# Kernel optimization log

Hardware: AMD Instinct MI355X
Metric: run time of the kernel (lower is better)

The kernel has to match this reference:

```python
import jax, jax.numpy as jnp
import numpy as np

# Kornia's fixed 5x5 pyramid (binomial) kernel used by build_pyramid/pyrdown
_PYR_K = np.array([[1, 4, 6, 4, 1],
                   [4, 16, 24, 16, 4],
                   [6, 24, 36, 24, 6],
                   [4, 16, 24, 16, 4],
                   [1, 4, 6, 4, 1]], dtype=np.float32) / 256.0


def _pyrdown(x):
    """kornia pyrdown: 5x5 binomial blur (reflect pad) + bilinear resize to (H//2, W//2)."""
    B, C, H, W = x.shape
    xp = jnp.pad(x, ((0, 0), (0, 0), (2, 2), (2, 2)), mode='reflect')
    k = jnp.broadcast_to(jnp.asarray(_PYR_K, x.dtype), (C, 1, 5, 5))  # depthwise
    y = jax.lax.conv_general_dilated(
        xp, k, window_strides=(1, 1), padding='VALID',
        feature_group_count=C, dimension_numbers=('NCHW', 'OIHW', 'NCHW'))
    # torch F.interpolate bilinear align_corners=False == jax resize bilinear, antialias off
    return jax.image.resize(y, (B, C, H // 2, W // 2), method='bilinear', antialias=False)


def _norm_pc(x):
    """Per-channel min-max normalization to [0,1] over spatial dims."""
    mx = jnp.max(x, axis=(2, 3), keepdims=True)
    mn = jnp.min(x, axis=(2, 3), keepdims=True)
    return (x - mn) / (mx - mn)


def _avg_local_max(x):
    """Mean of 16x16 tile maxima; torch loop range(0, H-16, 16) skips the last tile
    row/col, and with zero tiles the torch code yields nan_to_num(0/0) == 0."""
    B, C, H, W = x.shape
    s = 16
    ny = len(range(0, H - s, s))
    nx = len(range(0, W - s, s))
    if ny == 0 or nx == 0:
        return jnp.zeros((B, C, 1, 1), x.dtype)
    t = x[:, :, :ny * s, :nx * s].reshape(B, C, ny, s, nx, s)
    lmax = jnp.max(t, axis=(3, 5))           # [B,C,ny,nx]
    return jnp.mean(lmax, axis=(2, 3)).reshape(B, C, 1, 1)


def _sm_normalization(x):
    d = _norm_pc(x)
    lm = _avg_local_max(d)
    return d * (1.0 - lm) ** 2


def setup_inputs() -> dict:
    key = jax.random.key(0)
    x = jax.random.normal(key, (8, 3, 512, 512), dtype=jnp.float32)
    return {"x": x}


def reference(x):
    B, C, H, W = x.shape
    inp = _norm_pc(x)
    max_level = int(H).bit_length() - 1   # 9 for H=512
    u = max_level - 1

    # Gaussian pyramid of length max_level: [inp, pyrdown(inp), ...]
    pyr = [inp]
    for _ in range(max_level - 1):
        pyr.append(_pyrdown(pyr[-1]))

    acc = None
    for i in range(u - 1):
        h, w = pyr[i + 1].shape[2], pyr[i + 1].shape[3]
        up = jnp.repeat(jnp.repeat(pyr[i + 2], 2, axis=2), 2, axis=3)[:, :, :h, :w]
        d = jnp.abs(pyr[i + 1] - up)
        nd = jax.image.resize(_sm_normalization(d), (B, C, H, W),
                              method='bilinear', antialias=False)
        acc = nd if acc is None else acc + nd

    return jnp.mean(acc, axis=1)  # [B,H,W]
```

## Files before the change

kernel.cpp:

```cpp
#include <hip/hip_runtime.h>
#include <math.h>

#define NPLANES 24
#define FINF 3.402823466e38f

__host__ __device__ __forceinline__ int d_off(int li) {
    return 2097152 - (2097152 >> (2 * li));
}

__device__ __forceinline__ int refl(int v, int S) {
    if (v < 0) v = -v;
    if (v >= S) v = 2 * S - 2 - v;
    return v;
}

__device__ __forceinline__ float wmin64(float v) {
#pragma unroll
    for (int o = 32; o > 0; o >>= 1) v = fminf(v, __shfl_down(v, o, 64));
    return v;
}
__device__ __forceinline__ float wmax64(float v) {
#pragma unroll
    for (int o = 32; o > 0; o >>= 1) v = fmaxf(v, __shfl_down(v, o, 64));
    return v;
}
__device__ __forceinline__ float wsum64(float v) {
#pragma unroll
    for (int o = 32; o > 0; o >>= 1) v += __shfl_down(v, o, 64);
    return v;
}
__device__ __forceinline__ float bmin1024(float v, float* cross, int tid) {
    v = wmin64(v);
    if ((tid & 63) == 0) cross[tid >> 6] = v;
    __syncthreads();
    if (tid < 16) {
        float t = cross[tid];
#pragma unroll
        for (int o = 8; o > 0; o >>= 1) t = fminf(t, __shfl_down(t, o, 16));
        if (tid == 0) cross[0] = t;
    }
    __syncthreads();
    float r = cross[0];
    __syncthreads();
    return r;
}
__device__ __forceinline__ float bmax1024(float v, float* cross, int tid) {
    v = wmax64(v);
    if ((tid & 63) == 0) cross[tid >> 6] = v;
    __syncthreads();
    if (tid < 16) {
        float t = cross[tid];
#pragma unroll
        for (int o = 8; o > 0; o >>= 1) t = fmaxf(t, __shfl_down(t, o, 16));
        if (tid == 0) cross[0] = t;
    }
    __syncthreads();
    float r = cross[0];
    __syncthreads();
    return r;
}
__device__ __forceinline__ float bsum1024(float v, float* cross, int tid) {
    v = wsum64(v);
    if ((tid & 63) == 0) cross[tid >> 6] = v;
    __syncthreads();
    if (tid < 16) {
        float t = cross[tid];
#pragma unroll
        for (int o = 8; o > 0; o >>= 1) t += __shfl_down(t, o, 16);
        if (tid == 0) cross[0] = t;
    }
    __syncthreads();
    float r = cross[0];
    __syncthreads();
    return r;
}

__device__ __forceinline__ float stencil6(const float* s, int S, int i, int j) {
    const float w[6] = {1.f, 5.f, 10.f, 10.f, 5.f, 1.f};
    int rx[6];
#pragma unroll
    for (int b = 0; b < 6; ++b) rx[b] = refl(2 * j - 2 + b, S);
    float acc = 0.f;
#pragma unroll
    for (int a = 0; a < 6; ++a) {
        int ry = refl(2 * i - 2 + a, S);
        const float* rp = s + ry * S;
        float r = 0.f;
#pragma unroll
        for (int b = 0; b < 6; ++b) r += w[b] * rp[rx[b]];
        acc += w[a] * r;
    }
    return acc * (1.f / 1024.f);
}

template <int IS, bool HAS_D, int LI>
__global__ __launch_bounds__(256) void pyrdown_tiled(const float* __restrict__ in,
                                                     float* __restrict__ out,
                                                     float* __restrict__ dout,
                                                     float* __restrict__ tileMin,
                                                     float* __restrict__ tileMax) {
    constexpr int SO = IS / 2;
    constexpr int TO = 32;
    constexpr int TI = 2 * TO + 4;
    constexpr int TPA = SO / TO;
    __shared__ float sIn[TI * TI];
    __shared__ float sH[TI * TO];
    __shared__ float sOut[TO * TO];
    __shared__ float sD[HAS_D ? 64 * 65 : 1];
    __shared__ float rmn[HAS_D ? 256 : 1], rmx[HAS_D ? 256 : 1];

    const int tid = threadIdx.x;
    const int p = blockIdx.x / (TPA * TPA);
    const int t = blockIdx.x % (TPA * TPA);
    const int ty = t / TPA, tx = t % TPA;
    const int oy = ty * TO, ox = tx * TO;
    const int iy = 2 * oy - 2, ix = 2 * ox - 2;
    const float* ip = in + (size_t)p * IS * IS;

    for (int k = tid; k < TI * TI; k += 256) {
        int r = k / TI, c = k - r * TI;
        sIn[k] = ip[refl(iy + r, IS) * IS + refl(ix + c, IS)];
    }
    __syncthreads();

    for (int k = tid; k < TI * TO; k += 256) {
        int r = k / TO, j = k - r * TO;
        const float* rp = sIn + r * TI + 2 * j;
        sH[k] = rp[0] + 5.f * rp[1] + 10.f * rp[2] + 10.f * rp[3] + 5.f * rp[4] + rp[5];
    }
    __syncthreads();

    float* op = out + (size_t)p * SO * SO;
    for (int k = tid; k < TO * TO; k += 256) {
        int i = k / TO, j = k - i * TO;
        const float* cp = sH + (2 * i) * TO + j;
        float v = (cp[0] + 5.f * cp[TO] + 10.f * cp[2 * TO] + 10.f * cp[3 * TO] +
                   5.f * cp[4 * TO] + cp[5 * TO]) * (1.f / 1024.f);
        sOut[k] = v;
        op[(size_t)(oy + i) * SO + ox + j] = v;
    }

    if (HAS_D) {
        __syncthreads();
        float* dp = dout + (size_t)p * IS * IS;
        for (int k = tid; k < 4096; k += 256) {
            int yy = k >> 6, xx = k & 63;
            float dv = fabsf(sIn[(yy + 2) * TI + xx + 2] - sOut[(yy >> 1) * TO + (xx >> 1)]);
            sD[yy * 65 + xx] = dv;
            dp[(size_t)(2 * oy + yy) * IS + 2 * ox + xx] = dv;
        }
        __syncthreads();
        int s = tid >> 4, r = tid & 15;
        int tr = s >> 2, tc = s & 3;
        const float* rowp = sD + (tr * 16 + r) * 65 + tc * 16;
        float mn = FINF, mx = -FINF;
#pragma unroll
        for (int c = 0; c < 16; ++c) {
            float v = rowp[c];
            mn = fminf(mn, v); mx = fmaxf(mx, v);
        }
        rmn[tid] = mn; rmx[tid] = mx;
        __syncthreads();
        for (int st = 8; st > 0; st >>= 1) {
            if (r < st) {
                rmn[tid] = fminf(rmn[tid], rmn[tid + st]);
                rmx[tid] = fmaxf(rmx[tid], rmx[tid + st]);
            }
            __syncthreads();
        }
        if (r == 0) {
            constexpr int TA = IS / 16;
            constexpr int baseLi = (LI == 0) ? 0 : 6144;
            int gidx = baseLi + p * TA * TA + (ty * 4 + tr) * TA + (tx * 4 + tc);
            tileMin[gidx] = rmn[tid];
            tileMax[gidx] = rmx[tid];
        }
    }
}

__global__ __launch_bounds__(1024) void fused_small_kernel(const float* __restrict__ pyr3,
                                                           float* __restrict__ dBase,
                                                           const float* __restrict__ tileMin,
                                                           const float* __restrict__ tileMax,
                                                           float* __restrict__ A,
                                                           float* __restrict__ B) {
    __shared__ float sp3[4096], sd2[4096];
    __shared__ float sp4[1024], sd3[1024];
    __shared__ float sp5[256], sd4[256];
    __shared__ float sp6[64], sd5[64];
    __shared__ float sp7[16], sd6[16];
    __shared__ float cross[16];
    __shared__ float strip[256];
    __shared__ float tmaxLds[16];
    const int tid = threadIdx.x;
    const int p = blockIdx.x;

    ((float4*)sp3)[tid] = ((const float4*)(pyr3 + (size_t)p * 4096))[tid];
    __syncthreads();

    {
        float* d2g = dBase + d_off(2) + (size_t)p * 4096;
        int i = tid >> 5, j = tid & 31;
        float v = stencil6(sp3, 64, i, j);
        sp4[tid] = v;
#pragma unroll
        for (int di = 0; di < 2; ++di)
#pragma unroll
            for (int dj = 0; dj < 2; ++dj) {
                int y = 2 * i + di, x = 2 * j + dj;
                float dv = fabsf(sp3[y * 64 + x] - v);
                sd2[y * 64 + x] = dv;
                d2g[y * 64 + x] = dv;
            }
    }
    __syncthreads();
    if (tid < 256) {
        int i = tid >> 4, j = tid & 15;
        float v = stencil6(sp4, 32, i, j);
        sp5[tid] = v;
        float* d3g = dBase + d_off(3) + (size_t)p * 1024;
#pragma unroll
        for (int di = 0; di < 2; ++di)
#pragma unroll
            for (int dj = 0; dj < 2; ++dj) {
                int y = 2 * i + di, x = 2 * j + dj;
                float dv = fabsf(sp4[y * 32 + x] - v);
                sd3[y * 32 + x] = dv;
                d3g[y * 32 + x] = dv;
            }
    }
    __syncthreads();
    if (tid < 64) {
        int i = tid >> 3, j = tid & 7;
        float v = stencil6(sp5, 16, i, j);
        sp6[tid] = v;
        float* d4g = dBase + d_off(4) + (size_t)p * 256;
#pragma unroll
        for (int di = 0; di < 2; ++di)
#pragma unroll
            for (int dj = 0; dj < 2; ++dj) {
                int y = 2 * i + di, x = 2 * j + dj;
                float dv = fabsf(sp5[y * 16 + x] - v);
                sd4[y * 16 + x] = dv;
                d4g[y * 16 + x] = dv;
            }
    }
    __syncthreads();
    if (tid < 16) {
        int i = tid >> 2, j = tid & 3;
        float v = stencil6(sp6, 8, i, j);
        sp7[tid] = v;
        float* d5g = dBase + d_off(5) + (size_t)p * 64;
#pragma unroll
        for (int di = 0; di < 2; ++di)
#pragma unroll
            for (int dj = 0; dj < 2; ++dj) {
                int y = 2 * i + di, x = 2 * j + dj;
                float dv = fabsf(sp6[y * 8 + x] - v);
                sd5[y * 8 + x] = dv;
                d5g[y * 8 + x] = dv;
            }
    }
    __syncthreads();
    if (tid < 4) {
        int i = tid >> 1, j = tid & 1;
        float v = stencil6(sp7, 4, i, j);
        float* d6g = dBase + d_off(6) + (size_t)p * 16;
#pragma unroll
        for (int di = 0; di < 2; ++di)
#pragma unroll
            for (int dj = 0; dj < 2; ++dj) {
                int y = 2 * i + di, x = 2 * j + dj;
                float dv = fabsf(sp7[y * 4 + x] - v);
                sd6[y * 4 + x] = dv;
                d6g[y * 4 + x] = dv;
            }
    }
    __syncthreads();

    {
        float4 q = ((const float4*)sd2)[tid];
        float mn = fminf(fminf(q.x, q.y), fminf(q.z, q.w));
        float mx = fmaxf(fmaxf(q.x, q.y), fmaxf(q.z, q.w));
        mn = bmin1024(mn, cross, tid);
        mx = bmax1024(mx, cross, tid);
        if (tid < 256) {
            int t = tid >> 4, r = tid & 15;
            int ty = t >> 2, tx = t & 3;
            const float* rowp = sd2 + (ty * 16 + r) * 64 + tx * 16;
            float sm = -FINF;
#pragma unroll
            for (int c = 0; c < 16; ++c) sm = fmaxf(sm, rowp[c]);
            strip[tid] = sm;
        }
        __syncthreads();
        if (tid < 16) {
            float tm = -FINF;
            for (int r = 0; r < 16; ++r) tm = fmaxf(tm, strip[tid * 16 + r]);
            tmaxLds[tid] = tm;
        }
        __syncthreads();
        if (tid == 0) {
            float s = 0.f;
            for (int ty = 0; ty < 3; ++ty)
                for (int tx = 0; tx < 3; ++tx) s += tmaxLds[ty * 4 + tx];
            float inv = 1.f / (mx - mn);
            float lm = (s * (1.f / 9.f) - mn) * inv;
            float g = (1.f - lm) * (1.f - lm);
            A[2 * NPLANES + p] = g * inv;
            B[2 * NPLANES + p] = -mn * g * inv;
        }
        __syncthreads();
    }
    {
        float v = sd3[tid];
        float mn = bmin1024(v, cross, tid);
        float mx = bmax1024(v, cross, tid);
        float e = (tid < 256) ? sd3[(tid >> 4) * 32 + (tid & 15)] : -FINF;
        float tm = bmax1024(e, cross, tid);
        if (tid == 0) {
            float inv = 1.f / (mx - mn);
            float lm = (tm - mn) * inv;
            float g = (1.f - lm) * (1.f - lm);
            A[3 * NPLANES + p] = g * inv;
            B[3 * NPLANES + p] = -mn * g * inv;
        }
    }
    {
        float v = (tid < 256) ? sd4[tid] : FINF;
        float mn = bmin1024(v, cross, tid);
        v = (tid < 256) ? sd4[tid] : -FINF;
        float mx = bmax1024(v, cross, tid);
        if (tid == 0) {
            float inv = 1.f / (mx - mn);
            A[4 * NPLANES + p] = inv; B[4 * NPLANES + p] = -mn * inv;
        }
    }
    {
        float v = (tid < 64) ? sd5[tid] : FINF;
        float mn = bmin1024(v, cross, tid);
        v = (tid < 64) ? sd5[tid] : -FINF;
        float mx = bmax1024(v, cross, tid);
        if (tid == 0) {
            float inv = 1.f / (mx - mn);
            A[5 * NPLANES + p] = inv; B[5 * NPLANES + p] = -mn * inv;
        }
    }
    {
        float v = (tid < 16) ? sd6[tid] : FINF;
        float mn = bmin1024(v, cross, tid);
        v = (tid < 16) ? sd6[tid] : -FINF;
        float mx = bmax1024(v, cross, tid);
        if (tid == 0) {
            float inv = 1.f / (mx - mn);
            A[6 * NPLANES + p] = inv; B[6 * NPLANES + p] = -mn * inv;
        }
    }
    {
        float tmn = (tid < 256) ? tileMin[p * 256 + tid] : FINF;
        float tmx = (tid < 256) ? tileMax[p * 256 + tid] : -FINF;
        float mn = bmin1024(tmn, cross, tid);
        float mx = bmax1024(tmx, cross, tid);
        float su = (tid < 256 && (tid >> 4) < 15 && (tid & 15) < 15) ? tmx : 0.f;
        float sum = bsum1024(su, cross, tid);
        if (tid == 0) {
            float inv = 1.f / (mx - mn);
            float lm = (sum * (1.f / 225.f) - mn) * inv;
            float g = (1.f - lm) * (1.f - lm);
            A[0 * NPLANES + p] = g * inv;
            B[0 * NPLANES + p] = -mn * g * inv;
        }
    }
    {
        float tmn = (tid < 64) ? tileMin[6144 + p * 64 + tid] : FINF;
        float tmx = (tid < 64) ? tileMax[6144 + p * 64 + tid] : -FINF;
        float mn = bmin1024(tmn, cross, tid);
        float mx = bmax1024(tmx, cross, tid);
        float su = (tid < 64 && (tid >> 3) < 7 && (tid & 7) < 7) ? tmx : 0.f;
        float sum = bsum1024(su, cross, tid);
        if (tid == 0) {
            float inv = 1.f / (mx - mn);
            float lm = (sum * (1.f / 49.f) - mn) * inv;
            float g = (1.f - lm) * (1.f - lm);
            A[1 * NPLANES + p] = g * inv;
            B[1 * NPLANES + p] = -mn * g * inv;
        }
    }
}

__global__ __launch_bounds__(256) void final_kernel(const float* __restrict__ dBase,
                                                    const float* __restrict__ A,
                                                    const float* __restrict__ Bc,
                                                    float* __restrict__ out) {
    __shared__ float patch[1700];
    __shared__ float sBtot;
    const int tid = threadIdx.x;
    const int b = blockIdx.x >> 6;
    const int tile = blockIdx.x & 63;
    const int yb = (tile >> 3) << 6;
    const int xb = (tile & 7) << 6;

    if (tid == 0) {
        float s = 0.f;
        for (int k = 0; k < 7; ++k)
            for (int c = 0; c < 3; ++c) s += Bc[k * NPLANES + b * 3 + c];
        sBtot = s;
    }

    const int dims[7] = {34, 18, 10, 6, 4, 3, 3};
    const int lofs[7] = {0, 1156, 1480, 1580, 1616, 1632, 1641};
    int baseY[7], baseX[7];
#pragma unroll
    for (int li = 0; li < 7; ++li) {
        const int S = 256 >> li;
        const float s = 1.f / (float)(2 << li);
        baseY[li] = (int)floorf((yb + 0.5f) * s - 0.5f);
        baseX[li] = (int)floorf((xb + 0.5f) * s - 0.5f);
        const int dim = dims[li];
        const int n = dim * dim;
        const float* d0p = dBase + d_off(li) + (size_t)(b * 3) * S * S;
        const float* d1p = d0p + S * S;
        const float* d2p = d1p + S * S;
        const float A0 = A[li * NPLANES + b * 3 + 0];
        const float A1 = A[li * NPLANES + b * 3 + 1];
        const float A2 = A[li * NPLANES + b * 3 + 2];
        for (int k = tid; k < n; k += 256) {
            int r = k / dim, c = k - r * dim;
            int sr = min(max(baseY[li] + r, 0), S - 1);
            int sc = min(max(baseX[li] + c, 0), S - 1);
            int si = sr * S + sc;
            patch[lofs[li] + k] = A0 * d0p[si] + A1 * d1p[si] + A2 * d2p[si];
        }
    }
    __syncthreads();

    const int ty = tid >> 4, tx = tid & 15;
    const int gy0 = yb + (ty << 2), gx0 = xb + (tx << 2);
    float acc[4][4];
#pragma unroll
    for (int i = 0; i < 4; ++i)
#pragma unroll
        for (int j = 0; j < 4; ++j) acc[i][j] = 0.f;

    {
        const int dim = 34;
        float wy[4], wx[4];
        int ry[4], cx[4];
#pragma unroll
        for (int k = 0; k < 4; ++k) {
            float fy = (gy0 + k + 0.5f) * 0.5f - 0.5f;
            float fl = floorf(fy);
            wy[k] = fy - fl; ry[k] = (int)fl - baseY[0];
            float fx = (gx0 + k + 0.5f) * 0.5f - 0.5f;
            fl = floorf(fx);
            wx[k] = fx - fl; cx[k] = (int)fl - baseX[0];
        }
        const int r0 = ry[0], c0 = cx[0];
        const float* pp = patch + r0 * dim + c0;
        float P[4][4];
#pragma unroll
        for (int r = 0; r < 4; ++r)
#pragma unroll
            for (int c = 0; c < 4; ++c) P[r][c] = pp[r * dim + c];
        float h[4][4];
#pragma unroll
        for (int j = 0; j < 4; ++j) {
            int dx = cx[j] - c0;
#pragma unroll
            for (int r = 0; r < 4; ++r) {
                float a = dx == 0 ? P[r][0] : (dx == 1 ? P[r][1] : P[r][2]);
                float bb = dx == 0 ? P[r][1] : (dx == 1 ? P[r][2] : P[r][3]);
                h[r][j] = a + wx[j] * (bb - a);
            }
        }
#pragma unroll
        for (int i = 0; i < 4; ++i) {
            int dy = ry[i] - r0;
#pragma unroll
            for (int j = 0; j < 4; ++j) {
                float h0 = dy == 0 ? h[0][j] : (dy == 1 ? h[1][j] : h[2][j]);
                float h1 = dy == 0 ? h[1][j] : (dy == 1 ? h[2][j] : h[3][j]);
                acc[i][j] += h0 + wy[i] * (h1 - h0);
            }
        }
    }
#pragma unroll
    for (int li = 1; li < 7; ++li) {
        const int dim = dims[li];
        const float* P0 = patch + lofs[li];
        const float s = 1.f / (float)(2 << li);
        float wy[4], wx[4];
        int ry[4], cx[4];
#pragma unroll
        for (int k = 0; k < 4; ++k) {
            float fy = (gy0 + k + 0.5f) * s - 0.5f;
            float fl = floorf(fy);
            wy[k] = fy - fl; ry[k] = (int)fl - baseY[li];
            float fx = (gx0 + k + 0.5f) * s - 0.5f;
            fl = floorf(fx);
            wx[k] = fx - fl; cx[k] = (int)fl - baseX[li];
        }
        const int r0 = ry[0], c0 = cx[0];
        const float* pp = P0 + r0 * dim + c0;
        float P[3][3];
#pragma unroll
        for (int r = 0; r < 3; ++r)
#pragma unroll
            for (int c = 0; c < 3; ++c) P[r][c] = pp[r * dim + c];
        float h[3][4];
#pragma unroll
        for (int j = 0; j < 4; ++j) {
            int dx = cx[j] - c0;
#pragma unroll
            for (int r = 0; r < 3; ++r) {
                float a = dx == 0 ? P[r][0] : P[r][1];
                float bb = dx == 0 ? P[r][1] : P[r][2];
                h[r][j] = a + wx[j] * (bb - a);
            }
        }
#pragma unroll
        for (int i = 0; i < 4; ++i) {
            int dy = ry[i] - r0;
#pragma unroll
            for (int j = 0; j < 4; ++j) {
                float h0 = dy == 0 ? h[0][j] : h[1][j];
                float h1 = dy == 0 ? h[1][j] : h[2][j];
                acc[i][j] += h0 + wy[i] * (h1 - h0);
            }
        }
    }

    const float bt = sBtot;
    float* op = out + ((size_t)b * 512 + gy0) * 512 + gx0;
#pragma unroll
    for (int i = 0; i < 4; ++i) {
        float4 v;
        v.x = (acc[i][0] + bt) * (1.f / 3.f);
        v.y = (acc[i][1] + bt) * (1.f / 3.f);
        v.z = (acc[i][2] + bt) * (1.f / 3.f);
        v.w = (acc[i][3] + bt) * (1.f / 3.f);
        *(float4*)(op + (size_t)i * 512) = v;
    }
}

extern "C" void kernel_launch(void* const* d_in, const int* in_sizes, int n_in,
                              void* d_out, int out_size, void* d_ws, size_t ws_size,
                              hipStream_t stream) {
    (void)in_sizes; (void)n_in; (void)out_size; (void)ws_size;
    const float* x = (const float*)d_in[0];
    float* ws = (float*)d_ws;
    float* out = (float*)d_out;

    float* pyr1 = ws;
    float* pyr2 = ws + 1572864;
    float* pyr3 = ws + 1966080;
    float* dBase = ws + 2064384;
    float* tileMin = ws + 4161408;
    float* tileMax = ws + 4169088;
    float* A = ws + 4176768;
    float* Bc = ws + 4176936;

    pyrdown_tiled<512, false, 0><<<NPLANES * 64, 256, 0, stream>>>(x, pyr1, nullptr, nullptr, nullptr);
    pyrdown_tiled<256, true, 0><<<NPLANES * 16, 256, 0, stream>>>(pyr1, pyr2, dBase + d_off(0), tileMin, tileMax);
    pyrdown_tiled<128, true, 1><<<NPLANES * 4, 256, 0, stream>>>(pyr2, pyr3, dBase + d_off(1), tileMin, tileMax);
    fused_small_kernel<<<NPLANES, 1024, 0, stream>>>(pyr3, dBase, tileMin, tileMax, A, Bc);
    final_kernel<<<8 * 64, 256, 0, stream>>>(dBase, A, Bc, out);
}
```

Measured before the change: 119.3 us.

## Fuse level-2 pyrdown into the per-plane small kernel and vectorise stencil passes

Removes the separate 128x128 pyrdown launch and folds it into the per-plane fused kernel. That kernel now loads the whole 128x128 plane into shared memory and computes the level-3 pyramid, the level-1 difference map and its tile statistics there. The pyrdown_tiled horizontal and vertical passes are rewritten to use float4 shared-memory loads and stores. This saves one kernel launch and the pyr3 global round trip. The cost is heavier serial work in only 24 blocks of 1024 threads with about 115KB of LDS, which may lower parallelism for that stage.

New measurement: 116.5 us. -2.3%, faster.

```diff
diff --git a/kernel.cpp b/kernel.cpp
--- a/kernel.cpp
+++ b/kernel.cpp
@@ -93,7 +93,7 @@
     return acc * (1.f / 1024.f);
 }
 
-template <int IS, bool HAS_D, int LI>
+template <int IS, bool HAS_D>
 __global__ __launch_bounds__(256) void pyrdown_tiled(const float* __restrict__ in,
                                                      float* __restrict__ out,
                                                      float* __restrict__ dout,
@@ -123,21 +123,35 @@
     }
     __syncthreads();
 
-    for (int k = tid; k < TI * TO; k += 256) {
-        int r = k / TO, j = k - r * TO;
-        const float* rp = sIn + r * TI + 2 * j;
-        sH[k] = rp[0] + 5.f * rp[1] + 10.f * rp[2] + 10.f * rp[3] + 5.f * rp[4] + rp[5];
-    }
-    __syncthreads();
-
-    float* op = out + (size_t)p * SO * SO;
-    for (int k = tid; k < TO * TO; k += 256) {
-        int i = k / TO, j = k - i * TO;
-        const float* cp = sH + (2 * i) * TO + j;
-        float v = (cp[0] + 5.f * cp[TO] + 10.f * cp[2 * TO] + 10.f * cp[3 * TO] +
-                   5.f * cp[4 * TO] + cp[5 * TO]) * (1.f / 1024.f);
-        sOut[k] = v;
-        op[(size_t)(oy + i) * SO + ox + j] = v;
+    for (int k = tid; k < TI * 8; k += 256) {
+        int r = k >> 3, jq = k & 7;
+        const float4* rp = (const float4*)(sIn + r * TI + 8 * jq);
+        float4 v0 = rp[0], v1 = rp[1], v2 = rp[2];
+        float4 o;
+        o.x = v0.x + 5.f * v0.y + 10.f * v0.z + 10.f * v0.w + 5.f * v1.x + v1.y;
+        o.y = v0.z + 5.f * v0.w + 10.f * v1.x + 10.f * v1.y + 5.f * v1.z + v1.w;
+        o.z = v1.x + 5.f * v1.y + 10.f * v1.z + 10.f * v1.w + 5.f * v2.x + v2.y;
+        o.w = v1.z + 5.f * v1.w + 10.f * v2.x + 10.f * v2.y + 5.f * v2.z + v2.w;
+        *(float4*)(sH + r * TO + 4 * jq) = o;
+    }
+    __syncthreads();
+
+    {
+        int i = tid >> 3, jq = tid & 7;
+        const float* base = sH + (2 * i) * TO + 4 * jq;
+        float4 r0 = *(const float4*)(base);
+        float4 r1 = *(const float4*)(base + TO);
+        float4 r2 = *(const float4*)(base + 2 * TO);
+        float4 r3 = *(const float4*)(base + 3 * TO);
+        float4 r4 = *(const float4*)(base + 4 * TO);
+        float4 r5 = *(const float4*)(base + 5 * TO);
+        float4 o;
+        o.x = (r0.x + 5.f * r1.x + 10.f * r2.x + 10.f * r3.x + 5.f * r4.x + r5.x) * (1.f / 1024.f);
+        o.y = (r0.y + 5.f * r1.y + 10.f * r2.y + 10.f * r3.y + 5.f * r4.y + r5.y) * (1.f / 1024.f);
+        o.z = (r0.z + 5.f * r1.z + 10.f * r2.z + 10.f * r3.z + 5.f * r4.z + r5.z) * (1.f / 1024.f);
+        o.w = (r0.w + 5.f * r1.w + 10.f * r2.w + 10.f * r3.w + 5.f * r4.w + r5.w) * (1.f / 1024.f);
+        *(float4*)(sOut + i * TO + 4 * jq) = o;
+        *(float4*)(out + (size_t)p * SO * SO + (size_t)(oy + i) * SO + ox + 4 * jq) = o;
     }
 
     if (HAS_D) {
@@ -170,190 +184,110 @@
         }
         if (r == 0) {
             constexpr int TA = IS / 16;
-            constexpr int baseLi = (LI == 0) ? 0 : 6144;
-            int gidx = baseLi + p * TA * TA + (ty * 4 + tr) * TA + (tx * 4 + tc);
+            int gidx = p * TA * TA + (ty * 4 + tr) * TA + (tx * 4 + tc);
             tileMin[gidx] = rmn[tid];
             tileMax[gidx] = rmx[tid];
         }
     }
 }
 
-__global__ __launch_bounds__(1024) void fused_small_kernel(const float* __restrict__ pyr3,
+__global__ __launch_bounds__(1024) void fused_small_kernel(const float* __restrict__ pyr2,
                                                            float* __restrict__ dBase,
                                                            const float* __restrict__ tileMin,
                                                            const float* __restrict__ tileMax,
                                                            float* __restrict__ A,
                                                            float* __restrict__ B) {
-    __shared__ float sp3[4096], sd2[4096];
-    __shared__ float sp4[1024], sd3[1024];
-    __shared__ float sp5[256], sd4[256];
-    __shared__ float sp6[64], sd5[64];
-    __shared__ float sp7[16], sd6[16];
+    __shared__ float sP2[16384];
+    __shared__ float sHbuf[8192];
+    __shared__ float sP3[4096];
     __shared__ float cross[16];
-    __shared__ float strip[256];
-    __shared__ float tmaxLds[16];
+    __shared__ float strip[1024];
+    __shared__ float tmaxLds[64];
+    float* sd2 = sHbuf;
+    float* sp4 = sHbuf + 4096;
+    float* sd3 = sHbuf + 5120;
+    float* sp5 = sHbuf + 6144;
+    float* sd4 = sHbuf + 6400;
+    float* sp6 = sHbuf + 6656;
+    float* sd5 = sHbuf + 6720;
+    float* sp7 = sHbuf + 6784;
+    float* sd6 = sHbuf + 6800;
     const int tid = threadIdx.x;
     const int p = blockIdx.x;
 
-    ((float4*)sp3)[tid] = ((const float4*)(pyr3 + (size_t)p * 4096))[tid];
-    __syncthreads();
-
-    {
-        float* d2g = dBase + d_off(2) + (size_t)p * 4096;
-        int i = tid >> 5, j = tid & 31;
-        float v = stencil6(sp3, 64, i, j);
-        sp4[tid] = v;
-#pragma unroll
-        for (int di = 0; di < 2; ++di)
-#pragma unroll
-            for (int dj = 0; dj < 2; ++dj) {
-                int y = 2 * i + di, x = 2 * j + dj;
-                float dv = fabsf(sp3[y * 64 + x] - v);
-                sd2[y * 64 + x] = dv;
-                d2g[y * 64 + x] = dv;
-            }
-    }
-    __syncthreads();
-    if (tid < 256) {
-        int i = tid >> 4, j = tid & 15;
-        float v = stencil6(sp4, 32, i, j);
-        sp5[tid] = v;
-        float* d3g = dBase + d_off(3) + (size_t)p * 1024;
-#pragma unroll
-        for (int di = 0; di < 2; ++di)
-#pragma unroll
-            for (int dj = 0; dj < 2; ++dj) {
-                int y = 2 * i + di, x = 2 * j + dj;
-                float dv = fabsf(sp4[y * 32 + x] - v);
-                sd3[y * 32 + x] = dv;
-                d3g[y * 32 + x] = dv;
-            }
-    }
-    __syncthreads();
-    if (tid < 64) {
-        int i = tid >> 3, j = tid & 7;
-        float v = stencil6(sp5, 16, i, j);
-        sp6[tid] = v;
-        float* d4g = dBase + d_off(4) + (size_t)p * 256;
-#pragma unroll
-        for (int di = 0; di < 2; ++di)
-#pragma unroll
-            for (int dj = 0; dj < 2; ++dj) {
-                int y = 2 * i + di, x = 2 * j + dj;
-                float dv = fabsf(sp5[y * 16 + x] - v);
-                sd4[y * 16 + x] = dv;
-                d4g[y * 16 + x] = dv;
-            }
-    }
-    __syncthreads();
-    if (tid < 16) {
-        int i = tid >> 2, j = tid & 3;
-        float v = stencil6(sp6, 8, i, j);
-        sp7[tid] = v;
-        float* d5g = dBase + d_off(5) + (size_t)p * 64;
-#pragma unroll
-        for (int di = 0; di < 2; ++di)
-#pragma unroll
-            for (int dj = 0; dj < 2; ++dj) {
-                int y = 2 * i + di, x = 2 * j + dj;
-                float dv = fabsf(sp6[y * 8 + x] - v);
-                sd5[y * 8 + x] = dv;
-                d5g[y * 8 + x] = dv;
-            }
-    }
-    __syncthreads();
-    if (tid < 4) {
-        int i = tid >> 1, j = tid & 1;
-        float v = stencil6(sp7, 4, i, j);
-        float* d6g = dBase + d_off(6) + (size_t)p * 16;
-#pragma unroll
-        for (int di = 0; di < 2; ++di)
-#pragma unroll
-            for (int dj = 0; dj < 2; ++dj) {
-                int y = 2 * i + di, x = 2 * j + dj;
-                float dv = fabsf(sp7[y * 4 + x] - v);
-                sd6[y * 4 + x] = dv;
-                d6g[y * 4 + x] = dv;
-            }
-    }
-    __syncthreads();
-
-    {
-        float4 q = ((const float4*)sd2)[tid];
-        float mn = fminf(fminf(q.x, q.y), fminf(q.z, q.w));
-        float mx = fmaxf(fmaxf(q.x, q.y), fmaxf(q.z, q.w));
-        mn = bmin1024(mn, cross, tid);
-        mx = bmax1024(mx, cross, tid);
-        if (tid < 256) {
-            int t = tid >> 4, r = tid & 15;
-            int ty = t >> 2, tx = t & 3;
-            const float* rowp = sd2 + (ty * 16 + r) * 64 + tx * 16;
+    {
+        const float4* gp = (const float4*)(pyr2 + (size_t)p * 16384);
+        float4* sv = (float4*)sP2;
+        for (int k = tid; k < 4096; k += 1024) sv[k] = gp[k];
+    }
+    __syncthreads();
+    for (int k = tid; k < 8192; k += 1024) {
+        int r = k >> 6, c = k & 63;
+        int b0 = 2 * c - 2;
+        const float* rp = sP2 + r * 128;
+        sHbuf[k] = rp[refl(b0, 128)] + 5.f * rp[refl(b0 + 1, 128)] + 10.f * rp[refl(b0 + 2, 128)] +
+                   10.f * rp[refl(b0 + 3, 128)] + 5.f * rp[refl(b0 + 4, 128)] + rp[refl(b0 + 5, 128)];
+    }
+    __syncthreads();
+    for (int k = tid; k < 4096; k += 1024) {
+        int r3 = k >> 6, c = k & 63;
+        int b0 = 2 * r3 - 2;
+        float s = sHbuf[refl(b0, 128) * 64 + c] + 5.f * sHbuf[refl(b0 + 1, 128) * 64 + c] +
+                  10.f * sHbuf[refl(b0 + 2, 128) * 64 + c] + 10.f * sHbuf[refl(b0 + 3, 128) * 64 + c] +
+                  5.f * sHbuf[refl(b0 + 4, 128) * 64 + c] + sHbuf[refl(b0 + 5, 128) * 64 + c];
+        sP3[k] = s * (1.f / 1024.f);
+    }
+    __syncthreads();
+    float mnReg = FINF, mxReg = -FINF;
+    {
+        float4* d1g = (float4*)(dBase + d_off(1) + (size_t)p * 16384);
+        float4* sv = (float4*)sP2;
+        for (int k = tid; k < 4096; k += 1024) {
+            int row = k >> 5, c4 = k & 31;
+            float4 v = sv[k];
+            float2 o = *(const float2*)(sP3 + (row >> 1) * 64 + 2 * c4);
+            float4 dv;
+            dv.x = fabsf(v.x - o.x);
+            dv.y = fabsf(v.y - o.x);
+            dv.z = fabsf(v.z - o.y);
+            dv.w = fabsf(v.w - o.y);
+            sv[k] = dv;
+            d1g[k] = dv;
+            mnReg = fminf(mnReg, fminf(fminf(dv.x, dv.y), fminf(dv.z, dv.w)));
+            mxReg = fmaxf(mxReg, fmaxf(fmaxf(dv.x, dv.y), fmaxf(dv.z, dv.w)));
+        }
+    }
+    __syncthreads();
+    {
+        float mn = bmin1024(mnReg, cross, tid);
+        float mx = bmax1024(mxReg, cross, tid);
+        {
+            int s = tid >> 4, r = tid & 15;
+            int tr = s >> 3, tc = s & 7;
+            const float4* rowp = (const float4*)(sP2 + (tr * 16 + r) * 128 + tc * 16);
             float sm = -FINF;
 #pragma unroll
-            for (int c = 0; c < 16; ++c) sm = fmaxf(sm, rowp[c]);
+            for (int q = 0; q < 4; ++q) {
+                float4 v = rowp[q];
+                sm = fmaxf(sm, fmaxf(fmaxf(v.x, v.y), fmaxf(v.z, v.w)));
+            }
             strip[tid] = sm;
         }
         __syncthreads();
-        if (tid < 16) {
+        if (tid < 64) {
             float tm = -FINF;
             for (int r = 0; r < 16; ++r) tm = fmaxf(tm, strip[tid * 16 + r]);
             tmaxLds[tid] = tm;
         }
         __syncthreads();
-        if (tid == 0) {
-            float s = 0.f;
-            for (int ty = 0; ty < 3; ++ty)
-                for (int tx = 0; tx < 3; ++tx) s += tmaxLds[ty * 4 + tx];
-            float inv = 1.f / (mx - mn);
-            float lm = (s * (1.f / 9.f) - mn) * inv;
-            float g = (1.f - lm) * (1.f - lm);
-            A[2 * NPLANES + p] = g * inv;
-            B[2 * NPLANES + p] = -mn * g * inv;
-        }
-        __syncthreads();
-    }
-    {
-        float v = sd3[tid];
-        float mn = bmin1024(v, cross, tid);
-        float mx = bmax1024(v, cross, tid);
-        float e = (tid < 256) ? sd3[(tid >> 4) * 32 + (tid & 15)] : -FINF;
-        float tm = bmax1024(e, cross, tid);
+        float su = (tid < 64 && (tid >> 3) < 7 && (tid & 7) < 7) ? tmaxLds[tid] : 0.f;
+        float sum = bsum1024(su, cross, tid);
         if (tid == 0) {
             float inv = 1.f / (mx - mn);
-            float lm = (tm - mn) * inv;
+            float lm = (sum * (1.f / 49.f) - mn) * inv;
             float g = (1.f - lm) * (1.f - lm);
-            A[3 * NPLANES + p] = g * inv;
-            B[3 * NPLANES + p] = -mn * g * inv;
-        }
-    }
-    {
-        float v = (tid < 256) ? sd4[tid] : FINF;
-        float mn = bmin1024(v, cross, tid);
-        v = (tid < 256) ? sd4[tid] : -FINF;
-        float mx = bmax1024(v, cross, tid);
-        if (tid == 0) {
-            float inv = 1.f / (mx - mn);
-            A[4 * NPLANES + p] = inv; B[4 * NPLANES + p] = -mn * inv;
-        }
-    }
-    {
-        float v = (tid < 64) ? sd5[tid] : FINF;
-        float mn = bmin1024(v, cross, tid);
-        v = (tid < 64) ? sd5[tid] : -FINF;
-        float mx = bmax1024(v, cross, tid);
-        if (tid == 0) {
-            float inv = 1.f / (mx - mn);
-            A[5 * NPLANES + p] = inv; B[5 * NPLANES + p] = -mn * inv;
-        }
-    }
-    {
-        float v = (tid < 16) ? sd6[tid] : FINF;
-        float mn = bmin1024(v, cross, tid);
-        v = (tid < 16) ? sd6[tid] : -FINF;
-        float mx = bmax1024(v, cross, tid);
-        if (tid == 0) {
-            float inv = 1.f / (mx - mn);
-            A[6 * NPLANES + p] = inv; B[6 * NPLANES + p] = -mn * inv;
+            A[1 * NPLANES + p] = g * inv;
+            B[1 * NPLANES + p] = -mn * g * inv;
         }
     }
     {
@@ -371,19 +305,164 @@
             B[0 * NPLANES + p] = -mn * g * inv;
         }
     }
-    {
-        float tmn = (tid < 64) ? tileMin[6144 + p * 64 + tid] : FINF;
-        float tmx = (tid < 64) ? tileMax[6144 + p * 64 + tid] : -FINF;
-        float mn = bmin1024(tmn, cross, tid);
-        float mx = bmax1024(tmx, cross, tid);
-        float su = (tid < 64 && (tid >> 3) < 7 && (tid & 7) < 7) ? tmx : 0.f;
-        float sum = bsum1024(su, cross, tid);
+    __syncthreads();
+
+    {
+        float* d2g = dBase + d_off(2) + (size_t)p * 4096;
+        int i = tid >> 5, j = tid & 31;
+        float v = stencil6(sP3, 64, i, j);
+        sp4[tid] = v;
+#pragma unroll
+        for (int di = 0; di < 2; ++di)
+#pragma unroll
+            for (int dj = 0; dj < 2; ++dj) {
+                int y = 2 * i + di, x = 2 * j + dj;
+                float dv = fabsf(sP3[y * 64 + x] - v);
+                sd2[y * 64 + x] = dv;
+                d2g[y * 64 + x] = dv;
+            }
+    }
+    __syncthreads();
+    if (tid < 256) {
+        int i = tid >> 4, j = tid & 15;
+        float v = stencil6(sp4, 32, i, j);
+        sp5[tid] = v;
+        float* d3g = dBase + d_off(3) + (size_t)p * 1024;
+#pragma unroll
+        for (int di = 0; di < 2; ++di)
+#pragma unroll
+            for (int dj = 0; dj < 2; ++dj) {
+                int y = 2 * i + di, x = 2 * j + dj;
+                float dv = fabsf(sp4[y * 32 + x] - v);
+                sd3[y * 32 + x] = dv;
+                d3g[y * 32 + x] = dv;
+            }
+    }
+    __syncthreads();
+    if (tid < 64) {
+        int i = tid >> 3, j = tid & 7;
+        float v = stencil6(sp5, 16, i, j);
+        sp6[tid] = v;
+        float* d4g = dBase + d_off(4) + (size_t)p * 256;
+#pragma unroll
+        for (int di = 0; di < 2; ++di)
+#pragma unroll
+            for (int dj = 0; dj < 2; ++dj) {
+                int y = 2 * i + di, x = 2 * j + dj;
+                float dv = fabsf(sp5[y * 16 + x] - v);
+                sd4[y * 16 + x] = dv;
+                d4g[y * 16 + x] = dv;
+            }
+    }
+    __syncthreads();
+    if (tid < 16) {
+        int i = tid >> 2, j = tid & 3;
+        float v = stencil6(sp6, 8, i, j);
+        sp7[tid] = v;
+        float* d5g = dBase + d_off(5) + (size_t)p * 64;
+#pragma unroll
+        for (int di = 0; di < 2; ++di)
+#pragma unroll
+            for (int dj = 0; dj < 2; ++dj) {
+                int y = 2 * i + di, x = 2 * j + dj;
+                float dv = fabsf(sp6[y * 8 + x] - v);
+                sd5[y * 8 + x] = dv;
+                d5g[y * 8 + x] = dv;
+            }
+    }
+    __syncthreads();
+    if (tid < 4) {
+        int i = tid >> 1, j = tid & 1;
+        float v = stencil6(sp7, 4, i, j);
+        float* d6g = dBase + d_off(6) + (size_t)p * 16;
+#pragma unroll
+        for (int di = 0; di < 2; ++di)
+#pragma unroll
+            for (int dj = 0; dj < 2; ++dj) {
+                int y = 2 * i + di, x = 2 * j + dj;
+                float dv = fabsf(sp7[y * 4 + x] - v);
+                sd6[y * 4 + x] = dv;
+                d6g[y * 4 + x] = dv;
+            }
+    }
+    __syncthreads();
+
+    {
+        float4 q = ((const float4*)sd2)[tid];
+        float mn = fminf(fminf(q.x, q.y), fminf(q.z, q.w));
+        float mx = fmaxf(fmaxf(q.x, q.y), fmaxf(q.z, q.w));
+        mn = bmin1024(mn, cross, tid);
+        mx = bmax1024(mx, cross, tid);
+        if (tid < 256) {
+            int t = tid >> 4, r = tid & 15;
+            int ty = t >> 2, tx = t & 3;
+            const float* rowp = sd2 + (ty * 16 + r) * 64 + tx * 16;
+            float sm = -FINF;
+#pragma unroll
+            for (int c = 0; c < 16; ++c) sm = fmaxf(sm, rowp[c]);
+            strip[tid] = sm;
+        }
+        __syncthreads();
+        if (tid < 16) {
+            float tm = -FINF;
+            for (int r = 0; r < 16; ++r) tm = fmaxf(tm, strip[tid * 16 + r]);
+            tmaxLds[tid] = tm;
+        }
+        __syncthreads();
+        if (tid == 0) {
+            float s = 0.f;
+            for (int ty = 0; ty < 3; ++ty)
+                for (int tx = 0; tx < 3; ++tx) s += tmaxLds[ty * 4 + tx];
+            float inv = 1.f / (mx - mn);
+            float lm = (s * (1.f / 9.f) - mn) * inv;
+            float g = (1.f - lm) * (1.f - lm);
+            A[2 * NPLANES + p] = g * inv;
+            B[2 * NPLANES + p] = -mn * g * inv;
+        }
+        __syncthreads();
+    }
+    {
+        float v = sd3[tid];
+        float mn = bmin1024(v, cross, tid);
+        float mx = bmax1024(v, cross, tid);
+        float e = (tid < 256) ? sd3[(tid >> 4) * 32 + (tid & 15)] : -FINF;
+        float tm = bmax1024(e, cross, tid);
         if (tid == 0) {
             float inv = 1.f / (mx - mn);
-            float lm = (sum * (1.f / 49.f) - mn) * inv;
+            float lm = (tm - mn) * inv;
             float g = (1.f - lm) * (1.f - lm);
-            A[1 * NPLANES + p] = g * inv;
-            B[1 * NPLANES + p] = -mn * g * inv;
+            A[3 * NPLANES + p] = g * inv;
+            B[3 * NPLANES + p] = -mn * g * inv;
+        }
+    }
+    {
+        float v = (tid < 256) ? sd4[tid] : FINF;
+        float mn = bmin1024(v, cross, tid);
+        v = (tid < 256) ? sd4[tid] : -FINF;
+        float mx = bmax1024(v, cross, tid);
+        if (tid == 0) {
+            float inv = 1.f / (mx - mn);
+            A[4 * NPLANES + p] = inv; B[4 * NPLANES + p] = -mn * inv;
+        }
+    }
+    {
+        float v = (tid < 64) ? sd5[tid] : FINF;
+        float mn = bmin1024(v, cross, tid);
+        v = (tid < 64) ? sd5[tid] : -FINF;
+        float mx = bmax1024(v, cross, tid);
+        if (tid == 0) {
+            float inv = 1.f / (mx - mn);
+            A[5 * NPLANES + p] = inv; B[5 * NPLANES + p] = -mn * inv;
+        }
+    }
+    {
+        float v = (tid < 16) ? sd6[tid] : FINF;
+        float mn = bmin1024(v, cross, tid);
+        v = (tid < 16) ? sd6[tid] : -FINF;
+        float mx = bmax1024(v, cross, tid);
+        if (tid == 0) {
+            float inv = 1.f / (mx - mn);
+            A[6 * NPLANES + p] = inv; B[6 * NPLANES + p] = -mn * inv;
         }
     }
 }
@@ -553,16 +632,14 @@
 
     float* pyr1 = ws;
     float* pyr2 = ws + 1572864;
-    float* pyr3 = ws + 1966080;
-    float* dBase = ws + 2064384;
-    float* tileMin = ws + 4161408;
-    float* tileMax = ws + 4169088;
-    float* A = ws + 4176768;
-    float* Bc = ws + 4176936;
-
-    pyrdown_tiled<512, false, 0><<<NPLANES * 64, 256, 0, stream>>>(x, pyr1, nullptr, nullptr, nullptr);
-    pyrdown_tiled<256, true, 0><<<NPLANES * 16, 256, 0, stream>>>(pyr1, pyr2, dBase + d_off(0), tileMin, tileMax);
-    pyrdown_tiled<128, true, 1><<<NPLANES * 4, 256, 0, stream>>>(pyr2, pyr3, dBase + d_off(1), tileMin, tileMax);
-    fused_small_kernel<<<NPLANES, 1024, 0, stream>>>(pyr3, dBase, tileMin, tileMax, A, Bc);
+    float* dBase = ws + 1966080;
+    float* tileMin = ws + 4063104;
+    float* tileMax = ws + 4069248;
+    float* A = ws + 4075392;
+    float* Bc = ws + 4075560;
+
+    pyrdown_tiled<512, false><<<NPLANES * 64, 256, 0, stream>>>(x, pyr1, nullptr, nullptr, nullptr);
+    pyrdown_tiled<256, true><<<NPLANES * 16, 256, 0, stream>>>(pyr1, pyr2, dBase + d_off(0), tileMin, tileMax);
+    fused_small_kernel<<<NPLANES, 1024, 0, stream>>>(pyr2, dBase, tileMin, tileMax, A, Bc);
     final_kernel<<<8 * 64, 256, 0, stream>>>(dBase, A, Bc, out);
 }
```
